# Kernel optimization log

Measured on AMD Instinct MI355X. Metric: run time of the kernel, lower is better.

Reference implementation:

```python
import jax, jax.numpy as jnp
import numpy as np

IN_CH = 256
OUT_CH = 256
DIM = 8
HEADS = IN_CH // DIM            # 32
TOTAL = HEADS * DIM             # 256
C3 = 3 * TOTAL                  # 768
SCALES = (3, 5)
EPS = 1e-15


def _conv(x, w, b, groups=1, pad=0):
    # x: [B,C,H,W], w: [O, C//groups, kh, kw]
    y = jax.lax.conv_general_dilated(
        x, w, window_strides=(1, 1), padding=[(pad, pad), (pad, pad)],
        dimension_numbers=("NCHW", "OIHW", "NCHW"), feature_group_count=groups)
    return y + b[None, :, None, None]


def setup_inputs() -> dict:
    key = jax.random.key(0)
    ks = jax.random.split(key, 16)
    s = 0.02
    inp = {
        "x": jax.random.normal(ks[0], (8, IN_CH, 64, 64), jnp.float32),
        "qkv_w": jax.random.normal(ks[1], (C3, IN_CH, 1, 1), jnp.float32) * s,
        "qkv_b": jnp.zeros((C3,), jnp.float32),
        # scale 3: depthwise conv (groups=C3) then 1x1 grouped conv (groups=HEADS)
        "dw3_w": jax.random.normal(ks[2], (C3, 1, 3, 3), jnp.float32) * s,
        "dw3_b": jnp.zeros((C3,), jnp.float32),
        "pw3_w": jax.random.normal(ks[3], (C3, C3 // HEADS, 1, 1), jnp.float32) * s,
        "pw3_b": jnp.zeros((C3,), jnp.float32),
        # scale 5
        "dw5_w": jax.random.normal(ks[4], (C3, 1, 5, 5), jnp.float32) * s,
        "dw5_b": jnp.zeros((C3,), jnp.float32),
        "pw5_w": jax.random.normal(ks[5], (C3, C3 // HEADS, 1, 1), jnp.float32) * s,
        "pw5_b": jnp.zeros((C3,), jnp.float32),
        # proj: in = TOTAL*(1+len(SCALES)) = 768 -> OUT_CH
        "proj_w": jax.random.normal(ks[6], (OUT_CH, TOTAL * (1 + len(SCALES)), 1, 1), jnp.float32) * s,
        "proj_b": jnp.zeros((OUT_CH,), jnp.float32),
    }
    return inp


def _relu_linear_att(qkv):
    B, C, H, W = qkv.shape
    qkv = qkv.reshape(B, -1, 3 * DIM, H * W)          # [B, h, 3d, N]
    q = jax.nn.relu(qkv[:, :, :DIM])                   # [B, h, d, N]
    k = jax.nn.relu(qkv[:, :, DIM:2 * DIM])            # [B, h, d, N]
    v = qkv[:, :, 2 * DIM:]                            # [B, h, d, N]
    v = jnp.concatenate([v, jnp.ones_like(v[:, :, :1])], axis=2)  # pad ones -> [B,h,d+1,N]
    vk = jnp.einsum("bhdn,bhen->bhde", v, k)          # [B, h, d+1, d]
    out = jnp.einsum("bhde,bhen->bhdn", vk, q)        # [B, h, d+1, N]
    out = out[:, :, :-1] / (out[:, :, -1:] + EPS)      # normalize by denominator row
    return out.reshape(B, -1, H, W)


def reference(x, qkv_w, qkv_b, dw3_w, dw3_b, pw3_w, pw3_b,
              dw5_w, dw5_b, pw5_w, pw5_b, proj_w, proj_b):
    qkv = _conv(x, qkv_w, qkv_b)                                   # [B, 768, H, W]
    s3 = _conv(_conv(qkv, dw3_w, dw3_b, groups=C3, pad=1), pw3_w, pw3_b, groups=HEADS)
    s5 = _conv(_conv(qkv, dw5_w, dw5_b, groups=C3, pad=2), pw5_w, pw5_b, groups=HEADS)
    multi = jnp.concatenate([qkv, s3, s5], axis=1)                 # [B, 2304, H, W]
    att = _relu_linear_att(multi)                                  # [B, 768, H, W]
    return _conv(att, proj_w, proj_b)                              # [B, 256, H, W]
```

## Files before the change

kernel.cpp:

```cpp
#include <hip/hip_runtime.h>
#include <hip/hip_bf16.h>

#define C3 768
#define PIX 4096
#define NB 8

typedef __attribute__((ext_vector_type(8))) short bf16x8;
typedef __attribute__((ext_vector_type(4))) float f32x4;

__device__ __forceinline__ unsigned short f2bf(float f) {
    unsigned int u = __float_as_uint(f);
    u += 0x7fffu + ((u >> 16) & 1u);
    return (unsigned short)(u >> 16);
}
__device__ __forceinline__ float bf2f(unsigned short h) {
    return __uint_as_float((unsigned int)h << 16);
}

__device__ __forceinline__ void gload_lds16(const void* g, void* l) {
    __builtin_amdgcn_global_load_lds(
        (const __attribute__((address_space(1))) void*)g,
        (__attribute__((address_space(3))) void*)l, 16, 0, 0);
}

__global__ __launch_bounds__(256) void split3_kernel(
    const float* __restrict__ src, unsigned short* __restrict__ d,
    size_t stride, int n)
{
    int i = blockIdx.x * 256 + threadIdx.x;
    if (i < n) {
        float f = src[i];
        unsigned short h0 = f2bf(f);  float r1 = f - bf2f(h0);
        unsigned short h1 = f2bf(r1); float r2 = r1 - bf2f(h1);
        d[i]              = h0;
        d[i + stride]     = h1;
        d[i + 2 * stride] = f2bf(r2);
    }
}

__global__ __launch_bounds__(256) void split2_kernel(
    const float* __restrict__ src, unsigned short* __restrict__ d,
    size_t stride, int n)
{
    int i = blockIdx.x * 256 + threadIdx.x;
    if (i < n) {
        float f = src[i];
        unsigned short h0 = f2bf(f);
        d[i]          = h0;
        d[i + stride] = f2bf(f - bf2f(h0));
    }
}

__global__ __launch_bounds__(256) void transpose_split3_kernel(
    const float* __restrict__ src, unsigned short* __restrict__ d, size_t stride)
{
    __shared__ float t[32][33];
    const int b  = blockIdx.z;
    const int p0 = blockIdx.x * 32;
    const int k0 = blockIdx.y * 32;
    const int tx = threadIdx.x & 31, ty = threadIdx.x >> 5;

    const float* s = src + ((size_t)b * 256 + k0) * PIX + p0;
#pragma unroll
    for (int i = 0; i < 4; ++i)
        t[ty + i * 8][tx] = s[(size_t)(ty + i * 8) * PIX + tx];
    __syncthreads();
#pragma unroll
    for (int i = 0; i < 4; ++i) {
        const int p = ty + i * 8;
        float f = t[tx][p];
        unsigned short h0 = f2bf(f);  float r1 = f - bf2f(h0);
        unsigned short h1 = f2bf(r1); float r2 = r1 - bf2f(h1);
        size_t o = ((size_t)b * PIX + p0 + p) * 256 + k0 + tx;
        d[o]              = h0;
        d[o + stride]     = h1;
        d[o + 2 * stride] = f2bf(r2);
    }
}

template <int K, int S>
__global__ __launch_bounds__(256) void gemm_mfma_splitS(
    const unsigned short* __restrict__ A, const unsigned short* __restrict__ Bm,
    const float* __restrict__ bias, float* __restrict__ Y,
    int Mtiles, int M, size_t strideA, size_t strideB)
{
    __shared__ char lds[S * 24576];
    char* sA[S];
    char* sB[S];
#pragma unroll
    for (int s = 0; s < S; ++s) {
        sA[s] = lds + s * 16384;
        sB[s] = lds + S * 16384 + s * 8192;
    }

    const int nwg = gridDim.x;
    const int per = nwg >> 3;
    const int bid = blockIdx.x;
    const int wg  = (bid & 7) * per + (bid >> 3);
    const int tm  = wg % Mtiles;
    const int tn  = wg / Mtiles;
    const int bm  = tm * 128;
    const int gn0 = tn * 64;

    const int tid  = threadIdx.x;
    const int lane = tid & 63;
    const int wv   = tid >> 6;
    const int m0w  = (wv & 1) * 64;
    const int n0w  = (wv >> 1) * 32;

    const int l8  = lane >> 3;
    const int c16 = (lane & 7) * 16;
    const int gchunk = (c16 ^ (l8 << 4)) >> 1;
    const unsigned short* gA = A  + (size_t)(bm  + wv * 8 + l8) * K + gchunk;
    const unsigned short* gB = Bm + (size_t)(gn0 + wv * 8 + l8) * K + gchunk;
    const int ldsw = wv * 1024;

    f32x4 acc[4][2] = {};

    for (int k0 = 0; k0 < K; k0 += 64) {
        __syncthreads();
#pragma unroll
        for (int s = 0; s < S; ++s) {
#pragma unroll
            for (int j = 0; j < 4; ++j)
                gload_lds16(gA + s * strideA + (size_t)j * 32 * K + k0,
                            sA[s] + ldsw + j * 4096);
#pragma unroll
            for (int j = 0; j < 2; ++j)
                gload_lds16(gB + s * strideB + (size_t)j * 32 * K + k0,
                            sB[s] + ldsw + j * 4096);
        }
        __syncthreads();

#pragma unroll
        for (int kk = 0; kk < 2; ++kk) {
            const int kbyte = (kk * 32 + (lane >> 4) * 8) * 2;
            bf16x8 bfr[S][2];
#pragma unroll
            for (int ni = 0; ni < 2; ++ni) {
                const int r = n0w + ni * 16 + (lane & 15);
                const int byte = r * 128 + (kbyte ^ ((r & 7) << 4));
#pragma unroll
                for (int s = 0; s < S; ++s)
                    bfr[s][ni] = *(const bf16x8*)(sB[s] + byte);
            }
#pragma unroll
            for (int mi = 0; mi < 4; ++mi) {
                bf16x8 afr[S];
                const int r = m0w + mi * 16 + (lane & 15);
                const int byte = r * 128 + (kbyte ^ ((r & 7) << 4));
#pragma unroll
                for (int s = 0; s < S; ++s)
                    afr[s] = *(const bf16x8*)(sA[s] + byte);
#pragma unroll
                for (int ni = 0; ni < 2; ++ni) {
#pragma unroll
                    for (int i = 0; i < S; ++i)
#pragma unroll
                        for (int j = 0; j < S; ++j)
                            if (i + j < S)
                                acc[mi][ni] = __builtin_amdgcn_mfma_f32_16x16x32_bf16(
                                    afr[i], bfr[j][ni], acc[mi][ni], 0, 0, 0);
                }
            }
        }
    }

    const int b  = gn0 >> 12;
    const int p0 = gn0 & 4095;
#pragma unroll
    for (int mi = 0; mi < 4; ++mi)
#pragma unroll
        for (int ni = 0; ni < 2; ++ni) {
            const int p = p0 + n0w + ni * 16 + (lane & 15);
#pragma unroll
            for (int i = 0; i < 4; ++i) {
                const int m = bm + m0w + mi * 16 + (lane >> 4) * 4 + i;
                Y[((size_t)b * M + m) * PIX + p] = acc[mi][ni][i] + bias[m];
            }
        }
}

__global__ __launch_bounds__(256) void dwpw_kernel(
    const float* __restrict__ qkv,
    const float* __restrict__ w3,  const float* __restrict__ b3,
    const float* __restrict__ w5,  const float* __restrict__ b5,
    const float* __restrict__ pw3w, const float* __restrict__ pw3b,
    const float* __restrict__ pw5w, const float* __restrict__ pw5b,
    float* __restrict__ t3, float* __restrict__ t5)
{
    __shared__ float d3[24][260];
    __shared__ float d5[24][260];

    const int g  = blockIdx.y;
    const int b  = blockIdx.z;
    const int p  = blockIdx.x * 256 + threadIdx.x;
    const int h  = p >> 6, w = p & 63;
    const int c0 = g * 24;

    const float* src0 = qkv + ((size_t)b * C3 + c0) * PIX;

    for (int ic = 0; ic < 24; ++ic) {
        const int c = c0 + ic;
        const float* src = src0 + (size_t)ic * PIX;
        float k3[9], k5[25];
#pragma unroll
        for (int i = 0; i < 9; ++i)  k3[i] = w3[c * 9 + i];
#pragma unroll
        for (int i = 0; i < 25; ++i) k5[i] = w5[c * 25 + i];

        float acc3 = b3[c], acc5 = b5[c];
#pragma unroll
        for (int dy = -2; dy <= 2; ++dy) {
            const int hh = h + dy;
            const bool okY = ((unsigned)hh < 64u);
#pragma unroll
            for (int dx = -2; dx <= 2; ++dx) {
                const int ww = w + dx;
                float v = (okY && ((unsigned)ww < 64u)) ? src[hh * 64 + ww] : 0.f;
                acc5 = fmaf(k5[(dy + 2) * 5 + (dx + 2)], v, acc5);
                if (dy >= -1 && dy <= 1 && dx >= -1 && dx <= 1)
                    acc3 = fmaf(k3[(dy + 1) * 3 + (dx + 1)], v, acc3);
            }
        }
        d3[ic][threadIdx.x] = acc3;
        d5[ic][threadIdx.x] = acc5;
    }
    __syncthreads();

    float v3[24], v5[24];
#pragma unroll
    for (int ic = 0; ic < 24; ++ic) {
        v3[ic] = d3[ic][threadIdx.x];
        v5[ic] = d5[ic][threadIdx.x];
    }

    float* dst3 = t3 + ((size_t)b * C3 + c0) * PIX + p;
    float* dst5 = t5 + ((size_t)b * C3 + c0) * PIX + p;
#pragma unroll
    for (int co = 0; co < 24; ++co) {
        float a3 = pw3b[c0 + co], a5 = pw5b[c0 + co];
        const float* w3g = pw3w + (size_t)(c0 + co) * 24;
        const float* w5g = pw5w + (size_t)(c0 + co) * 24;
#pragma unroll
        for (int ic = 0; ic < 24; ++ic) {
            a3 = fmaf(w3g[ic], v3[ic], a3);
            a5 = fmaf(w5g[ic], v5[ic], a5);
        }
        dst3[(size_t)co * PIX] = a3;
        dst5[(size_t)co * PIX] = a5;
    }
}

__global__ __launch_bounds__(256) void vk_reduce_kernel(
    const float* __restrict__ qkv, const float* __restrict__ s3,
    const float* __restrict__ s5, float* __restrict__ vkout)
{
    const int hh = blockIdx.x;
    const int b  = blockIdx.y;
    const float* src = (hh < 32) ? qkv : ((hh < 64) ? s3 : s5);
    const int ch0 = (hh & 31) * 24;
    const float* base = src + ((size_t)b * C3 + ch0) * PIX;

    float acc[9][8] = {};
    for (int p = threadIdx.x; p < PIX; p += 256) {
        float kk[8], vv[8];
#pragma unroll
        for (int e = 0; e < 8; ++e) kk[e] = fmaxf(base[(8 + e) * PIX + p], 0.f);
#pragma unroll
        for (int d = 0; d < 8; ++d) vv[d] = base[(16 + d) * PIX + p];
#pragma unroll
        for (int d = 0; d < 8; ++d)
#pragma unroll
            for (int e = 0; e < 8; ++e)
                acc[d][e] = fmaf(vv[d], kk[e], acc[d][e]);
#pragma unroll
        for (int e = 0; e < 8; ++e) acc[8][e] += kk[e];
    }

#pragma unroll
    for (int i = 0; i < 9; ++i)
#pragma unroll
        for (int j = 0; j < 8; ++j) {
            float s = acc[i][j];
            for (int off = 32; off; off >>= 1) s += __shfl_down(s, off, 64);
            acc[i][j] = s;
        }

    __shared__ float red[4][72];
    const int wave = threadIdx.x >> 6, lane = threadIdx.x & 63;
    if (lane == 0) {
#pragma unroll
        for (int i = 0; i < 9; ++i)
#pragma unroll
            for (int j = 0; j < 8; ++j) red[wave][i * 8 + j] = acc[i][j];
    }
    __syncthreads();
    const int t = threadIdx.x;
    if (t < 72) {
        float s = red[0][t] + red[1][t] + red[2][t] + red[3][t];
        vkout[((size_t)b * 96 + hh) * 72 + t] = s;
    }
}

__global__ __launch_bounds__(256) void att_apply_kernel(
    const float* __restrict__ qkv, const float* __restrict__ s3,
    const float* __restrict__ s5, const float* __restrict__ vkin,
    unsigned short* __restrict__ aT, size_t stride)
{
    const int hh = blockIdx.y;
    const int b  = blockIdx.z;
    const int p  = blockIdx.x * 256 + threadIdx.x;

    __shared__ float vk[72];
    if (threadIdx.x < 72)
        vk[threadIdx.x] = vkin[((size_t)b * 96 + hh) * 72 + threadIdx.x];
    __syncthreads();

    const float* src = (hh < 32) ? qkv : ((hh < 64) ? s3 : s5);
    const int ch0 = (hh & 31) * 24;
    const float* base = src + ((size_t)b * C3 + ch0) * PIX + p;

    float q[8];
#pragma unroll
    for (int e = 0; e < 8; ++e) q[e] = fmaxf(base[(size_t)e * PIX], 0.f);

    float den = 0.f;
#pragma unroll
    for (int e = 0; e < 8; ++e) den = fmaf(vk[64 + e], q[e], den);
    const float inv = 1.f / (den + 1e-15f);

    union { unsigned short u[8]; uint4 v; } H, L;
#pragma unroll
    for (int d = 0; d < 8; ++d) {
        float num = 0.f;
#pragma unroll
        for (int e = 0; e < 8; ++e) num = fmaf(vk[d * 8 + e], q[e], num);
        float o = num * inv;
        unsigned short h = f2bf(o);
        H.u[d] = h;
        L.u[d] = f2bf(o - bf2f(h));
    }
    const size_t row = (size_t)b * PIX + p;
    *(uint4*)(aT + row * C3 + hh * 8) = H.v;
    *(uint4*)(aT + stride + row * C3 + hh * 8) = L.v;
}

extern "C" void kernel_launch(void* const* d_in, const int* in_sizes, int n_in,
                              void* d_out, int out_size, void* d_ws, size_t ws_size,
                              hipStream_t stream)
{
    const float* x      = (const float*)d_in[0];
    const float* qkv_w  = (const float*)d_in[1];
    const float* qkv_b  = (const float*)d_in[2];
    const float* dw3_w  = (const float*)d_in[3];
    const float* dw3_b  = (const float*)d_in[4];
    const float* pw3_w  = (const float*)d_in[5];
    const float* pw3_b  = (const float*)d_in[6];
    const float* dw5_w  = (const float*)d_in[7];
    const float* dw5_b  = (const float*)d_in[8];
    const float* pw5_w  = (const float*)d_in[9];
    const float* pw5_b  = (const float*)d_in[10];
    const float* proj_w = (const float*)d_in[11];
    const float* proj_b = (const float*)d_in[12];
    float* out = (float*)d_out;

    const size_t SZb = (size_t)C3 * PIX;
    const size_t XTb = (size_t)256 * PIX;
    const int    NW  = C3 * 256;

    const size_t wbytes = (3 + 2) * (size_t)NW * 2;

    int cb = NB;
    while (cb > 1) {
        size_t need = wbytes +
                      (size_t)cb * (3 * SZb * 4 + 3 * XTb * 2 + 2 * SZb * 2 +
                                    (size_t)96 * 72 * 4);
        if (need <= ws_size) break;
        cb >>= 1;
    }

    char* wp = (char*)d_ws;
    unsigned short* WQ = (unsigned short*)wp;   wp += 3 * (size_t)NW * 2;
    unsigned short* WP = (unsigned short*)wp;   wp += 2 * (size_t)NW * 2;
    float* qkv = (float*)wp;                    wp += (size_t)cb * SZb * 4;
    float* t3  = (float*)wp;                    wp += (size_t)cb * SZb * 4;
    float* t5  = (float*)wp;                    wp += (size_t)cb * SZb * 4;
    unsigned short* xT = (unsigned short*)wp;   wp += 3 * (size_t)cb * XTb * 2;
    unsigned short* aT = (unsigned short*)wp;   wp += 2 * (size_t)cb * SZb * 2;
    float* vkb = (float*)wp;

    const size_t strideXT = (size_t)cb * XTb;
    const size_t strideAT = (size_t)cb * SZb;

    split3_kernel<<<(NW + 255) / 256, 256, 0, stream>>>(qkv_w, WQ, (size_t)NW, NW);
    split2_kernel<<<(NW + 255) / 256, 256, 0, stream>>>(proj_w, WP, (size_t)NW, NW);

    for (int b0 = 0; b0 < NB; b0 += cb) {
        const float* xb = x   + (size_t)b0 * 256 * PIX;
        float*       ob = out + (size_t)b0 * 256 * PIX;

        transpose_split3_kernel<<<dim3(128, 8, cb), 256, 0, stream>>>(xb, xT, strideXT);

        gemm_mfma_splitS<256, 3><<<dim3(6 * cb * 64), 256, 0, stream>>>(
            WQ, xT, qkv_b, qkv, 6, C3, (size_t)NW, strideXT);

        dwpw_kernel<<<dim3(16, 32, cb), 256, 0, stream>>>(
            qkv, dw3_w, dw3_b, dw5_w, dw5_b,
            pw3_w, pw3_b, pw5_w, pw5_b, t3, t5);

        vk_reduce_kernel<<<dim3(96, cb), 256, 0, stream>>>(qkv, t3, t5, vkb);

        att_apply_kernel<<<dim3(16, 96, cb), 256, 0, stream>>>(
            qkv, t3, t5, vkb, aT, strideAT);

        gemm_mfma_splitS<768, 2><<<dim3(2 * cb * 64), 256, 0, stream>>>(
            WP, aT, proj_b, ob, 2, 256, (size_t)NW, strideAT);
    }
}
```

Baseline: 553.4 us.

## Stage depthwise input rows in double-buffered LDS halo tiles and accumulate pointwise outputs in registers

The depthwise 3x3/5x5 stage now loads each channel's 8x68 halo tile (4 rows plus a 2-pixel border) into shared memory, double-buffered so the next channel is staged while the current one is computed. This replaces per-thread bounds-checked global loads of 25 neighbours. The grouped pointwise conv is folded into the channel loop, accumulating 48 outputs per thread in registers instead of staging depthwise results through a large LDS array. This cuts redundant global reads and LDS footprint, but adds a barrier per channel and more register pressure.

Result: slower. 578.2 us (+4.5%).

```diff
diff --git a/kernel.cpp b/kernel.cpp
--- a/kernel.cpp
+++ b/kernel.cpp
@@ -189,66 +189,75 @@
     const float* __restrict__ pw5w, const float* __restrict__ pw5b,
     float* __restrict__ t3, float* __restrict__ t5)
 {
-    __shared__ float d3[24][260];
-    __shared__ float d5[24][260];
-
-    const int g  = blockIdx.y;
-    const int b  = blockIdx.z;
-    const int p  = blockIdx.x * 256 + threadIdx.x;
-    const int h  = p >> 6, w = p & 63;
-    const int c0 = g * 24;
+    __shared__ float tile[2][8][68];
+
+    const int g   = blockIdx.y;
+    const int b   = blockIdx.z;
+    const int tid = threadIdx.x;
+    const int p   = blockIdx.x * 256 + tid;
+    const int r0  = blockIdx.x * 4;
+    const int c0  = g * 24;
+    const int lr  = tid >> 6;
+    const int lc  = tid & 63;
 
     const float* src0 = qkv + ((size_t)b * C3 + c0) * PIX;
 
+    float o3[24], o5[24];
+#pragma unroll
+    for (int co = 0; co < 24; ++co) {
+        o3[co] = pw3b[c0 + co];
+        o5[co] = pw5b[c0 + co];
+    }
+
+    auto stage = [&](int ic, int buf) {
+        const float* src = src0 + (size_t)ic * PIX;
+#pragma unroll
+        for (int e = tid; e < 544; e += 256) {
+            const int rr = e / 68, cc = e % 68;
+            const int gr = r0 - 2 + rr, gc = cc - 2;
+            float v = 0.f;
+            if ((unsigned)gr < 64u && (unsigned)gc < 64u) v = src[gr * 64 + gc];
+            tile[buf][rr][cc] = v;
+        }
+    };
+
+    stage(0, 0);
     for (int ic = 0; ic < 24; ++ic) {
+        __syncthreads();
+        if (ic + 1 < 24) stage(ic + 1, (ic + 1) & 1);
+
         const int c = c0 + ic;
-        const float* src = src0 + (size_t)ic * PIX;
-        float k3[9], k5[25];
-#pragma unroll
-        for (int i = 0; i < 9; ++i)  k3[i] = w3[c * 9 + i];
-#pragma unroll
-        for (int i = 0; i < 25; ++i) k5[i] = w5[c * 25 + i];
+        const float* k5 = w5 + c * 25;
+        const float* k3 = w3 + c * 9;
+        const float (*T)[68] = tile[ic & 1];
 
         float acc3 = b3[c], acc5 = b5[c];
 #pragma unroll
-        for (int dy = -2; dy <= 2; ++dy) {
-            const int hh = h + dy;
-            const bool okY = ((unsigned)hh < 64u);
-#pragma unroll
-            for (int dx = -2; dx <= 2; ++dx) {
-                const int ww = w + dx;
-                float v = (okY && ((unsigned)ww < 64u)) ? src[hh * 64 + ww] : 0.f;
-                acc5 = fmaf(k5[(dy + 2) * 5 + (dx + 2)], v, acc5);
-                if (dy >= -1 && dy <= 1 && dx >= -1 && dx <= 1)
-                    acc3 = fmaf(k3[(dy + 1) * 3 + (dx + 1)], v, acc3);
+        for (int dy = 0; dy < 5; ++dy) {
+#pragma unroll
+            for (int dx = 0; dx < 5; ++dx) {
+                const float v = T[lr + dy][lc + dx];
+                acc5 = fmaf(k5[dy * 5 + dx], v, acc5);
+                if (dy >= 1 && dy <= 3 && dx >= 1 && dx <= 3)
+                    acc3 = fmaf(k3[(dy - 1) * 3 + (dx - 1)], v, acc3);
             }
         }
-        d3[ic][threadIdx.x] = acc3;
-        d5[ic][threadIdx.x] = acc5;
-    }
-    __syncthreads();
-
-    float v3[24], v5[24];
-#pragma unroll
-    for (int ic = 0; ic < 24; ++ic) {
-        v3[ic] = d3[ic][threadIdx.x];
-        v5[ic] = d5[ic][threadIdx.x];
+
+        const float* w3g = pw3w + (size_t)c0 * 24 + ic;
+        const float* w5g = pw5w + (size_t)c0 * 24 + ic;
+#pragma unroll
+        for (int co = 0; co < 24; ++co) {
+            o3[co] = fmaf(w3g[co * 24], acc3, o3[co]);
+            o5[co] = fmaf(w5g[co * 24], acc5, o5[co]);
+        }
     }
 
     float* dst3 = t3 + ((size_t)b * C3 + c0) * PIX + p;
     float* dst5 = t5 + ((size_t)b * C3 + c0) * PIX + p;
 #pragma unroll
     for (int co = 0; co < 24; ++co) {
-        float a3 = pw3b[c0 + co], a5 = pw5b[c0 + co];
-        const float* w3g = pw3w + (size_t)(c0 + co) * 24;
-        const float* w5g = pw5w + (size_t)(c0 + co) * 24;
-#pragma unroll
-        for (int ic = 0; ic < 24; ++ic) {
-            a3 = fmaf(w3g[ic], v3[ic], a3);
-            a5 = fmaf(w5g[ic], v5[ic], a5);
-        }
-        dst3[(size_t)co * PIX] = a3;
-        dst5[(size_t)co * PIX] = a5;
+        dst3[(size_t)co * PIX] = o3[co];
+        dst5[(size_t)co * PIX] = o5[co];
     }
 }
 
```
